# Kernel optimization log

Measured on AMD Instinct MI355X. Metric: run time of the kernel, lower is better.

The kernel has to match this reference:

```python
import jax, jax.numpy as jnp
import numpy as np

N_NODES = 100000
N_EDGES = 1600000
N_FEAT = 128
N_GRAPHS = 256
N_CLASSES = 2
BN_EPS = 1e-5


def _glorot(key, shape):
    lim = float(np.sqrt(6.0 / (shape[0] + shape[1])))
    return jax.random.uniform(key, shape, jnp.float32, -lim, lim)


def setup_inputs() -> dict:
    key = jax.random.key(0)
    ks = jax.random.split(key, 16)
    x = jax.random.normal(ks[0], (N_NODES, N_FEAT), jnp.float32)
    edge_index = jax.random.randint(ks[1], (2, N_EDGES), 0, N_NODES, jnp.int64)
    batch = jnp.sort(jax.random.randint(ks[2], (N_NODES,), 0, N_GRAPHS, jnp.int64))
    dims = [(N_FEAT, 16), (16, 32), (32, 64), (64, 50)]
    params = {}
    for i, (di, do) in enumerate(dims):
        params[f"W{i+1}"] = _glorot(ks[3 + i], (di, do))
        params[f"b{i+1}"] = jnp.zeros((do,), jnp.float32)
    params["bn_gamma"] = jnp.ones((50,), jnp.float32)
    params["bn_beta"] = jnp.zeros((50,), jnp.float32)
    params["fc1_W"] = _glorot(ks[8], (50, 30))
    params["fc1_b"] = jnp.zeros((30,), jnp.float32)
    params["fc2_W"] = _glorot(ks[9], (30, 20))
    params["fc2_b"] = jnp.zeros((20,), jnp.float32)
    params["fc3_W"] = _glorot(ks[10], (20, N_CLASSES))
    params["fc3_b"] = jnp.zeros((N_CLASSES,), jnp.float32)
    return {"x": x, "edge_index": edge_index, "batch": batch, **params}


def _gcn(x, W, b, src, dst):
    # GCNConv with normalize=False: out_i = sum_{(j->i) in E} (x_j @ W) + b
    h = x @ W                                   # [N, d_out]
    agg = jax.ops.segment_sum(h[src], dst, num_segments=N_NODES)
    return agg + b


def reference(x, edge_index, batch,
              W1, b1, W2, b2, W3, b3, W4, b4,
              bn_gamma, bn_beta,
              fc1_W, fc1_b, fc2_W, fc2_b, fc3_W, fc3_b):
    src, dst = edge_index[0], edge_index[1]
    lrelu = lambda v: jax.nn.leaky_relu(v, 0.01)
    h = lrelu(_gcn(x, W1, b1, src, dst))
    h = lrelu(_gcn(h, W2, b2, src, dst))
    h = lrelu(_gcn(h, W3, b3, src, dst))
    h = _gcn(h, W4, b4, src, dst)
    # BatchNorm over the node dimension (training-style batch stats, biased var)
    mu = jnp.mean(h, axis=0)
    var = jnp.mean((h - mu) ** 2, axis=0)
    h = lrelu((h - mu) * jax.lax.rsqrt(var + BN_EPS) * bn_gamma + bn_beta)
    # global_add_pool over graphs
    g = jax.ops.segment_sum(h, batch, num_segments=N_GRAPHS)   # [G, 50]
    g = lrelu(g @ fc1_W + fc1_b)   # dropout inactive (eval)
    g = lrelu(g @ fc2_W + fc2_b)
    g = g @ fc3_W + fc3_b
    return jax.nn.log_softmax(g, axis=-1)
```

## Files before the change

### kernel.cpp

```cpp
#include <hip/hip_runtime.h>

#define N_NODES 100000
#define N_EDGES 1600000
#define N_GRAPHS 256
#define NBKT 196
#define BKT_CAP 16384
#define BCHUNKS 391
#define MM1_BLOCKS 3125
#define A_BLOCKS (BCHUNKS + MM1_BLOCKS)

__device__ __forceinline__ float lrelu(float v) { return v > 0.f ? v : 0.01f * v; }

__device__ __forceinline__ unsigned short f2bf(float f) {
    unsigned int u = __float_as_uint(f);
    return (unsigned short)((u + 0x7FFFu + ((u >> 16) & 1u)) >> 16);
}
__device__ __forceinline__ float bf2f(unsigned short h) {
    return __uint_as_float(((unsigned int)h) << 16);
}
__device__ __forceinline__ float blo(unsigned int v) { return __uint_as_float(v << 16); }
__device__ __forceinline__ float bhi(unsigned int v) { return __uint_as_float(v & 0xFFFF0000u); }

__global__ void bucket_and_mm1(const int* __restrict__ src, const int* __restrict__ dst,
                               int* __restrict__ bucketCnt, unsigned int* __restrict__ bkt,
                               const float* __restrict__ x, const float* __restrict__ W1,
                               unsigned short* __restrict__ T1) {
    __shared__ float lds[32 * 132 + 128 * 16];
    int bid = blockIdx.x;
    int tid = threadIdx.x;
    if (bid % 9 == 0) {
        int* lcnt = (int*)lds;
        int* loff = lcnt + 784;
        int* lcnt2 = loff + 784;
        int fi = bid / 9;
        for (int i = tid; i < 784; i += 256) { lcnt[i] = 0; lcnt2[i] = 0; }
        __syncthreads();
        int sub = tid & 3;
        int e0 = fi * 4096 + tid;
        int dcache[16], scache[16];
#pragma unroll
        for (int i = 0; i < 16; ++i) {
            int e = e0 + i * 256;
            if (e < N_EDGES) {
                dcache[i] = dst[e];
                scache[i] = src[e];
                atomicAdd(&lcnt[sub * 196 + (dcache[i] >> 9)], 1);
            }
        }
        __syncthreads();
        if (tid < NBKT) {
            int c0 = lcnt[tid], c1 = lcnt[196 + tid], c2 = lcnt[392 + tid], c3 = lcnt[588 + tid];
            int tot = c0 + c1 + c2 + c3;
            int goff = (tot > 0) ? atomicAdd(&bucketCnt[tid], tot) : 0;
            loff[tid] = goff;
            loff[196 + tid] = goff + c0;
            loff[392 + tid] = goff + c0 + c1;
            loff[588 + tid] = goff + c0 + c1 + c2;
        }
        __syncthreads();
#pragma unroll
        for (int i = 0; i < 16; ++i) {
            int e = e0 + i * 256;
            if (e < N_EDGES) {
                int d = dcache[i];
                int b = d >> 9;
                int pos = loff[sub * 196 + b] + atomicAdd(&lcnt2[sub * 196 + b], 1);
                if (pos < BKT_CAP)
                    bkt[(size_t)b * BKT_CAP + pos] =
                        ((unsigned int)(d & 511) << 17) | (unsigned int)scache[i];
            }
        }
    } else {
        int mb = bid - bid / 9 - 1;
        float* xs = lds;
        float* wsm = lds + 32 * 132;
        const int n0 = mb * 32;
        for (int i = tid; i < 128 * 16; i += 256) wsm[i] = W1[i];
        const float4* X4 = (const float4*)x;
        for (int i = tid; i < 32 * 32; i += 256) {
            int r2 = i >> 5, c = i & 31;
            ((float4*)(xs + r2 * 132))[c] = X4[(size_t)(n0 + r2) * 32 + c];
        }
        __syncthreads();
        int r2 = tid >> 3, jp = tid & 7;
        float a0 = 0.f, a1 = 0.f;
        const float4* xr4 = (const float4*)(xs + r2 * 132);
#pragma unroll
        for (int k4 = 0; k4 < 32; ++k4) {
            float4 xv = xr4[k4];
            float2 w0 = *(const float2*)(wsm + (4 * k4 + 0) * 16 + 2 * jp);
            float2 w1 = *(const float2*)(wsm + (4 * k4 + 1) * 16 + 2 * jp);
            float2 w2 = *(const float2*)(wsm + (4 * k4 + 2) * 16 + 2 * jp);
            float2 w3 = *(const float2*)(wsm + (4 * k4 + 3) * 16 + 2 * jp);
            a0 = fmaf(xv.x, w0.x, a0); a1 = fmaf(xv.x, w0.y, a1);
            a0 = fmaf(xv.y, w1.x, a0); a1 = fmaf(xv.y, w1.y, a1);
            a0 = fmaf(xv.z, w2.x, a0); a1 = fmaf(xv.z, w2.y, a1);
            a0 = fmaf(xv.w, w3.x, a0); a1 = fmaf(xv.w, w3.y, a1);
        }
        ((unsigned int*)T1)[(size_t)(n0 + r2) * 8 + jp] = ((unsigned int)f2bf(a1) << 16) | f2bf(a0);
    }
}

__global__ void build_bucket(const unsigned int* __restrict__ bkt, const int* __restrict__ bucketCnt,
                             int* __restrict__ base, int* __restrict__ adj) {
    __shared__ int ldeg[512];
    __shared__ int lofs[512];
    __shared__ int ssum[256];
    int b = blockIdx.x;
    int tid = threadIdx.x;
    ssum[tid] = (tid < NBKT) ? bucketCnt[tid] : 0;
    __syncthreads();
    for (int off = 1; off < 256; off <<= 1) {
        int add = (tid >= off) ? ssum[tid - off] : 0;
        __syncthreads();
        ssum[tid] += add;
        __syncthreads();
    }
    int gbase = (b > 0) ? ssum[b - 1] : 0;
    int cnt = min(((b < NBKT) ? bucketCnt[b] : 0), BKT_CAP);
    int nstart = b * 512;
    int nn = min(512, N_NODES - nstart);
    const unsigned int* seg = bkt + (size_t)b * BKT_CAP;
    for (int i = tid; i < 512; i += 256) ldeg[i] = 0;
    __syncthreads();
    for (int e = tid; e < cnt; e += 256) atomicAdd(&ldeg[seg[e] >> 17], 1);
    __syncthreads();
    int a0 = ldeg[2 * tid], a1 = ldeg[2 * tid + 1];
    __syncthreads();
    ssum[tid] = a0 + a1;
    __syncthreads();
    for (int off = 1; off < 256; off <<= 1) {
        int add = (tid >= off) ? ssum[tid - off] : 0;
        __syncthreads();
        ssum[tid] += add;
        __syncthreads();
    }
    int prev = (tid > 0) ? ssum[tid - 1] : 0;
    lofs[2 * tid] = prev;
    lofs[2 * tid + 1] = prev + a0;
    __syncthreads();
    for (int i = tid; i < nn; i += 256) base[nstart + i] = gbase + lofs[i];
    if (b == 0 && tid == 0) base[N_NODES] = N_EDGES;
    for (int i = tid; i < 512; i += 256) ldeg[i] = 0;
    __syncthreads();
    for (int e = tid; e < cnt; e += 256) {
        unsigned int v = seg[e];
        int dl = (int)(v >> 17);
        int pos = atomicAdd(&ldeg[dl], 1);
        adj[gbase + lofs[dl] + pos] = (int)(v & 0x1FFFFu);
    }
}

template <int DIN, int DOUT, int ROWS, bool BIAS, bool RELU>
__global__ void matmul_rt(const unsigned int* __restrict__ X2, const float* __restrict__ W,
                          unsigned short* __restrict__ T, const float* __restrict__ bias) {
    constexpr int PAIRS = DOUT / 2;
    constexpr int PT = (PAIRS + 3) / 4;
    constexpr int RT = ROWS / 4;
    constexpr int XST = DIN + 1;
    __shared__ float xs[ROWS * XST];
    __shared__ float wsm[DIN * DOUT + 8];
    const int n0 = blockIdx.x * ROWS;
    const bool full = (n0 + ROWS <= N_NODES);
    int tid = threadIdx.x;
    for (int i = tid; i < DIN * DOUT; i += 256) wsm[i] = W[i];
    constexpr int V = DIN / 2;
    for (int i = tid; i < ROWS * V; i += 256) {
        int r = i / V, c = i - r * V;
        int node = n0 + r;
        unsigned int v = (full || node < N_NODES) ? X2[(size_t)node * V + c] : 0u;
        xs[r * XST + 2 * c]     = blo(v);
        xs[r * XST + 2 * c + 1] = bhi(v);
    }
    __syncthreads();
    if (tid >= RT * PT) return;
    int rt = tid / PT, pt = tid - rt * PT;
    const float* xr0 = xs + (rt * 4) * XST;
    const float* wp = wsm + 2 * (pt * 4);
    float2 acc[4][4];
#pragma unroll
    for (int i = 0; i < 4; ++i)
#pragma unroll
        for (int j = 0; j < 4; ++j) acc[i][j] = make_float2(0.f, 0.f);
#pragma unroll 4
    for (int k = 0; k < DIN; ++k) {
        float xv0 = xr0[k];
        float xv1 = xr0[XST + k];
        float xv2 = xr0[2 * XST + k];
        float xv3 = xr0[3 * XST + k];
        const float* wr = wp + k * DOUT;
        float2 w0 = *(const float2*)(wr);
        float2 w1 = *(const float2*)(wr + 2);
        float2 w2 = *(const float2*)(wr + 4);
        float2 w3 = *(const float2*)(wr + 6);
        acc[0][0].x = fmaf(xv0, w0.x, acc[0][0].x); acc[0][0].y = fmaf(xv0, w0.y, acc[0][0].y);
        acc[0][1].x = fmaf(xv0, w1.x, acc[0][1].x); acc[0][1].y = fmaf(xv0, w1.y, acc[0][1].y);
        acc[0][2].x = fmaf(xv0, w2.x, acc[0][2].x); acc[0][2].y = fmaf(xv0, w2.y, acc[0][2].y);
        acc[0][3].x = fmaf(xv0, w3.x, acc[0][3].x); acc[0][3].y = fmaf(xv0, w3.y, acc[0][3].y);
        acc[1][0].x = fmaf(xv1, w0.x, acc[1][0].x); acc[1][0].y = fmaf(xv1, w0.y, acc[1][0].y);
        acc[1][1].x = fmaf(xv1, w1.x, acc[1][1].x); acc[1][1].y = fmaf(xv1, w1.y, acc[1][1].y);
        acc[1][2].x = fmaf(xv1, w2.x, acc[1][2].x); acc[1][2].y = fmaf(xv1, w2.y, acc[1][2].y);
        acc[1][3].x = fmaf(xv1, w3.x, acc[1][3].x); acc[1][3].y = fmaf(xv1, w3.y, acc[1][3].y);
        acc[2][0].x = fmaf(xv2, w0.x, acc[2][0].x); acc[2][0].y = fmaf(xv2, w0.y, acc[2][0].y);
        acc[2][1].x = fmaf(xv2, w1.x, acc[2][1].x); acc[2][1].y = fmaf(xv2, w1.y, acc[2][1].y);
        acc[2][2].x = fmaf(xv2, w2.x, acc[2][2].x); acc[2][2].y = fmaf(xv2, w2.y, acc[2][2].y);
        acc[2][3].x = fmaf(xv2, w3.x, acc[2][3].x); acc[2][3].y = fmaf(xv2, w3.y, acc[2][3].y);
        acc[3][0].x = fmaf(xv3, w0.x, acc[3][0].x); acc[3][0].y = fmaf(xv3, w0.y, acc[3][0].y);
        acc[3][1].x = fmaf(xv3, w1.x, acc[3][1].x); acc[3][1].y = fmaf(xv3, w1.y, acc[3][1].y);
        acc[3][2].x = fmaf(xv3, w2.x, acc[3][2].x); acc[3][2].y = fmaf(xv3, w2.y, acc[3][2].y);
        acc[3][3].x = fmaf(xv3, w3.x, acc[3][3].x); acc[3][3].y = fmaf(xv3, w3.y, acc[3][3].y);
    }
    unsigned int* Tu = (unsigned int*)T;
#pragma unroll
    for (int i = 0; i < 4; ++i) {
        int node = n0 + rt * 4 + i;
        if (full || node < N_NODES) {
#pragma unroll
            for (int j = 0; j < 4; ++j) {
                int jp = pt * 4 + j;
                if (PAIRS % 4 == 0 || jp < PAIRS) {
                    float a0 = acc[i][j].x, a1 = acc[i][j].y;
                    if (BIAS) { a0 += bias[2 * jp]; a1 += bias[2 * jp + 1]; }
                    if (RELU) { a0 = lrelu(a0); a1 = lrelu(a1); }
                    Tu[(size_t)node * PAIRS + jp] = ((unsigned int)f2bf(a1) << 16) | f2bf(a0);
                }
            }
        }
    }
}

template <int DOUT, bool BIAS, bool RELU>
__global__ void gather_agg_bf16(const unsigned short* __restrict__ T, const int* __restrict__ base,
                                const int* __restrict__ adj, const float* __restrict__ b,
                                unsigned short* __restrict__ out) {
    constexpr int PAIRS = DOUT / 2;
    int gi = blockIdx.x * 256 + threadIdx.x;
    int node = gi / PAIRS;
    int j = gi - node * PAIRS;
    if (node >= N_NODES) return;
    const unsigned int* Tu = (const unsigned int*)T;
    int e0 = base[node], e1 = base[node + 1];
    float a0 = 0.f, a1 = 0.f, c0 = 0.f, c1 = 0.f;
    int k = e0;
    for (; k + 7 < e1; k += 8) {
        int s0 = adj[k], s1 = adj[k + 1], s2 = adj[k + 2], s3 = adj[k + 3];
        int s4 = adj[k + 4], s5 = adj[k + 5], s6 = adj[k + 6], s7 = adj[k + 7];
        unsigned int v0 = Tu[(size_t)s0 * PAIRS + j];
        unsigned int v1 = Tu[(size_t)s1 * PAIRS + j];
        unsigned int v2 = Tu[(size_t)s2 * PAIRS + j];
        unsigned int v3 = Tu[(size_t)s3 * PAIRS + j];
        unsigned int v4 = Tu[(size_t)s4 * PAIRS + j];
        unsigned int v5 = Tu[(size_t)s5 * PAIRS + j];
        unsigned int v6 = Tu[(size_t)s6 * PAIRS + j];
        unsigned int v7 = Tu[(size_t)s7 * PAIRS + j];
        a0 += blo(v0); a1 += bhi(v0);
        c0 += blo(v1); c1 += bhi(v1);
        a0 += blo(v2); a1 += bhi(v2);
        c0 += blo(v3); c1 += bhi(v3);
        a0 += blo(v4); a1 += bhi(v4);
        c0 += blo(v5); c1 += bhi(v5);
        a0 += blo(v6); a1 += bhi(v6);
        c0 += blo(v7); c1 += bhi(v7);
    }
    for (; k + 3 < e1; k += 4) {
        int s0 = adj[k], s1 = adj[k + 1], s2 = adj[k + 2], s3 = adj[k + 3];
        unsigned int v0 = Tu[(size_t)s0 * PAIRS + j];
        unsigned int v1 = Tu[(size_t)s1 * PAIRS + j];
        unsigned int v2 = Tu[(size_t)s2 * PAIRS + j];
        unsigned int v3 = Tu[(size_t)s3 * PAIRS + j];
        a0 += blo(v0); a1 += bhi(v0);
        c0 += blo(v1); c1 += bhi(v1);
        a0 += blo(v2); a1 += bhi(v2);
        c0 += blo(v3); c1 += bhi(v3);
    }
    for (; k < e1; ++k) {
        int s = adj[k];
        unsigned int v = Tu[(size_t)s * PAIRS + j];
        a0 += blo(v); a1 += bhi(v);
    }
    a0 += c0; a1 += c1;
    if (BIAS) { a0 += b[2 * j]; a1 += b[2 * j + 1]; }
    if (RELU) { a0 = lrelu(a0); a1 = lrelu(a1); }
    ((unsigned int*)out)[(size_t)node * PAIRS + j] = ((unsigned int)f2bf(a1) << 16) | f2bf(a0);
}

__global__ void bn_partial_kernel(const unsigned short* __restrict__ H, float* __restrict__ sum,
                                  float* __restrict__ ssum) {
    int tid = threadIdx.x;
    int j = tid % 50;
    int sub = tid / 50;
    float s = 0.f, ss = 0.f;
    if (tid < 250) {
        for (int node = blockIdx.x * 5 + sub; node < N_NODES; node += gridDim.x * 5) {
            float v = bf2f(H[(size_t)node * 50 + j]);
            s += v;
            ss += v * v;
        }
    }
    __shared__ float ls[256], lss[256];
    ls[tid] = s;
    lss[tid] = ss;
    __syncthreads();
    if (tid < 50) {
        float a = ls[tid] + ls[tid + 50] + ls[tid + 100] + ls[tid + 150] + ls[tid + 200];
        float c = lss[tid] + lss[tid + 50] + lss[tid + 100] + lss[tid + 150] + lss[tid + 200];
        atomicAdd(&sum[tid], a);
        atomicAdd(&ssum[tid], c);
    }
}

__global__ void setup_kernel(const int* __restrict__ batch, int* __restrict__ bounds,
                             int* __restrict__ bucketCnt, float* __restrict__ bnsum,
                             float* __restrict__ bnssum) {
    int tid = threadIdx.x;
    if (blockIdx.x == 0) {
        bucketCnt[tid] = 0;
    } else if (tid < 64) {
        bnsum[tid] = 0.f;
        bnssum[tid] = 0.f;
    }
    int g = blockIdx.x * 256 + tid;
    if (g > N_GRAPHS) return;
    int lo = 0, hi = N_NODES;
    while (lo < hi) {
        int mid = (lo + hi) >> 1;
        if (batch[mid] < g) lo = mid + 1; else hi = mid;
    }
    bounds[g] = lo;
}

__global__ void pool_seg_kernel(const unsigned short* __restrict__ H, const int* __restrict__ bounds,
                                const float* __restrict__ bnsum, const float* __restrict__ bnssum,
                                const float* __restrict__ gamma, const float* __restrict__ beta,
                                float* __restrict__ G) {
    int g = blockIdx.x;
    int s = bounds[g], e = bounds[g + 1];
    int tid = threadIdx.x;
    int j = tid % 50;
    int sub = tid / 50;
    float acc = 0.f;
    if (tid < 250) {
        float m = bnsum[j] / (float)N_NODES;
        float var = bnssum[j] / (float)N_NODES - m * m;
        float rs = rsqrtf(fmaxf(var, 0.f) + 1e-5f);
        float scale = rs * gamma[j];
        float shift = beta[j] - m * scale;
        for (int n = s + sub; n < e; n += 5) {
            float v = fmaf(bf2f(H[(size_t)n * 50 + j]), scale, shift);
            acc += lrelu(v);
        }
    }
    __shared__ float ls[256];
    ls[tid] = acc;
    __syncthreads();
    if (tid < 50) {
        G[g * 50 + tid] = ls[tid] + ls[tid + 50] + ls[tid + 100] + ls[tid + 150] + ls[tid + 200];
    }
}

__global__ void mlp_kernel(const float* __restrict__ G,
                           const float* __restrict__ fc1W, const float* __restrict__ fc1b,
                           const float* __restrict__ fc2W, const float* __restrict__ fc2b,
                           const float* __restrict__ fc3W, const float* __restrict__ fc3b,
                           float* __restrict__ out) {
    __shared__ float lw[2192];
    int tid = threadIdx.x;
    for (int i = tid; i < 1500; i += 256) lw[i] = fc1W[i];
    for (int i = tid; i < 30; i += 256) lw[1500 + i] = fc1b[i];
    for (int i = tid; i < 600; i += 256) lw[1530 + i] = fc2W[i];
    for (int i = tid; i < 20; i += 256) lw[2130 + i] = fc2b[i];
    for (int i = tid; i < 40; i += 256) lw[2150 + i] = fc3W[i];
    for (int i = tid; i < 2; i += 256) lw[2190 + i] = fc3b[i];
    __syncthreads();
    int g = blockIdx.x * 32 + tid;
    if (tid >= 32 || g >= N_GRAPHS) return;
    float a[50];
#pragma unroll
    for (int k = 0; k < 50; ++k) a[k] = G[g * 50 + k];
    float h1[30];
#pragma unroll
    for (int j = 0; j < 30; ++j) {
        float acc = lw[1500 + j];
#pragma unroll
        for (int k = 0; k < 50; ++k) acc = fmaf(a[k], lw[k * 30 + j], acc);
        h1[j] = lrelu(acc);
    }
    float h2[20];
#pragma unroll
    for (int j = 0; j < 20; ++j) {
        float acc = lw[2130 + j];
#pragma unroll
        for (int k = 0; k < 30; ++k) acc = fmaf(h1[k], lw[1530 + k * 20 + j], acc);
        h2[j] = lrelu(acc);
    }
    float z0 = lw[2190], z1 = lw[2191];
#pragma unroll
    for (int k = 0; k < 20; ++k) {
        z0 = fmaf(h2[k], lw[2150 + k * 2 + 0], z0);
        z1 = fmaf(h2[k], lw[2150 + k * 2 + 1], z1);
    }
    float m = fmaxf(z0, z1);
    float lse = m + logf(expf(z0 - m) + expf(z1 - m));
    out[g * 2 + 0] = z0 - lse;
    out[g * 2 + 1] = z1 - lse;
}

extern "C" void kernel_launch(void* const* d_in, const int* in_sizes, int n_in,
                              void* d_out, int out_size, void* d_ws, size_t ws_size,
                              hipStream_t stream) {
    const float* x     = (const float*)d_in[0];
    const int*   ei    = (const int*)d_in[1];
    const int*   batch = (const int*)d_in[2];
    const float* W1 = (const float*)d_in[3];  const float* b1 = (const float*)d_in[4];
    const float* W2 = (const float*)d_in[5];  const float* b2 = (const float*)d_in[6];
    const float* W3 = (const float*)d_in[7];  const float* b3 = (const float*)d_in[8];
    const float* W4 = (const float*)d_in[9];  const float* b4 = (const float*)d_in[10];
    const float* bng = (const float*)d_in[11]; const float* bnb = (const float*)d_in[12];
    const float* fc1W = (const float*)d_in[13]; const float* fc1b = (const float*)d_in[14];
    const float* fc2W = (const float*)d_in[15]; const float* fc2b = (const float*)d_in[16];
    const float* fc3W = (const float*)d_in[17]; const float* fc3b = (const float*)d_in[18];

    const int* src = ei;
    const int* dst = ei + N_EDGES;

    char* w = (char*)d_ws;
    unsigned short* bufA = (unsigned short*)w;      w += (size_t)6400000 * 2;
    unsigned short* bufB = (unsigned short*)w;      w += (size_t)6400000 * 2;
    int*   adj  = (int*)w;                          w += (size_t)N_EDGES * 4;
    unsigned int* bkt = (unsigned int*)w;           w += (size_t)NBKT * BKT_CAP * 4;
    int*   base = (int*)w;                          w += (size_t)(N_NODES + 1) * 4;
    int*   bucketCnt = (int*)w;                     w += 256 * 4;
    float* bnsum = (float*)w;                       w += 64 * 4;
    float* bnssum = (float*)w;                      w += 64 * 4;
    int*   bounds = (int*)w;                        w += (N_GRAPHS + 1) * 4;
    float* G    = (float*)w;                        w += (size_t)N_GRAPHS * 50 * 4;

    dim3 blk(256);

    setup_kernel<<<2, 256, 0, stream>>>(batch, bounds, bucketCnt, bnsum, bnssum);

    bucket_and_mm1<<<A_BLOCKS, blk, 0, stream>>>(src, dst, bucketCnt, bkt, x, W1, bufA);

    build_bucket<<<NBKT, blk, 0, stream>>>(bkt, bucketCnt, base, adj);

    gather_agg_bf16<16, true, true><<<(N_NODES * 8 + 255) / 256, blk, 0, stream>>>(bufA, base, adj, b1, bufB);

    gather_agg_bf16<16, false, false><<<(N_NODES * 8 + 255) / 256, blk, 0, stream>>>(bufB, base, adj, nullptr, bufA);
    matmul_rt<16, 32, 256, true, true><<<(N_NODES + 255) / 256, blk, 0, stream>>>((const unsigned int*)bufA, W2, bufB, b2);

    gather_agg_bf16<32, false, false><<<(N_NODES * 16 + 255) / 256, blk, 0, stream>>>(bufB, base, adj, nullptr, bufA);
    matmul_rt<32, 64, 128, true, true><<<(N_NODES + 127) / 128, blk, 0, stream>>>((const unsigned int*)bufA, W3, bufB, b3);

    matmul_rt<64, 50, 128, false, false><<<(N_NODES + 127) / 128, blk, 0, stream>>>((const unsigned int*)bufB, W4, bufA, nullptr);
    gather_agg_bf16<50, true, false><<<(N_NODES * 25 + 255) / 256, blk, 0, stream>>>(bufA, base, adj, b4, bufB);

    bn_partial_kernel<<<256, blk, 0, stream>>>(bufB, bnsum, bnssum);

    pool_seg_kernel<<<N_GRAPHS, blk, 0, stream>>>(bufB, bounds, bnsum, bnssum, bng, bnb, G);

    mlp_kernel<<<8, 256, 0, stream>>>(G, fc1W, fc1b, fc2W, fc2b, fc3W, fc3b, (float*)d_out);
}
```

Measured before the change: 282.3 us.

## Overlap the first matmul with CSR build instead of edge bucketing; unroll gather deeper

Edge bucketing now runs alone in its own kernel with smaller per-block chunks, twice as many blocks. The first-layer matmul is interleaved with the per-bucket CSR build (one build block every 17), so the dense matmul hides the latency of the atomic-heavy build step. The gather kernel's main loop now issues 16 neighbour loads per iteration instead of 8 to raise memory-level parallelism, at the cost of more registers. Kernel count stays the same, but the work is split differently across the first two launches.

```diff
diff --git a/kernel.cpp b/kernel.cpp
--- a/kernel.cpp
+++ b/kernel.cpp
@@ -5,9 +5,9 @@
 #define N_GRAPHS 256
 #define NBKT 196
 #define BKT_CAP 16384
-#define BCHUNKS 391
+#define B_BLOCKS 782
 #define MM1_BLOCKS 3125
-#define A_BLOCKS (BCHUNKS + MM1_BLOCKS)
+#define BM_BLOCKS (NBKT + MM1_BLOCKS)
 
 __device__ __forceinline__ float lrelu(float v) { return v > 0.f ? v : 0.01f * v; }
 
@@ -21,57 +21,105 @@
 __device__ __forceinline__ float blo(unsigned int v) { return __uint_as_float(v << 16); }
 __device__ __forceinline__ float bhi(unsigned int v) { return __uint_as_float(v & 0xFFFF0000u); }
 
-__global__ void bucket_and_mm1(const int* __restrict__ src, const int* __restrict__ dst,
-                               int* __restrict__ bucketCnt, unsigned int* __restrict__ bkt,
-                               const float* __restrict__ x, const float* __restrict__ W1,
-                               unsigned short* __restrict__ T1) {
+__global__ void bucket_only(const int* __restrict__ src, const int* __restrict__ dst,
+                            int* __restrict__ bucketCnt, unsigned int* __restrict__ bkt) {
+    __shared__ int lcnt[784], loff[784], lcnt2[784];
+    int fi = blockIdx.x;
+    int tid = threadIdx.x;
+    for (int i = tid; i < 784; i += 256) { lcnt[i] = 0; lcnt2[i] = 0; }
+    __syncthreads();
+    int sub = tid & 3;
+    int e0 = fi * 2048 + tid;
+    int dcache[8], scache[8];
+#pragma unroll
+    for (int i = 0; i < 8; ++i) {
+        int e = e0 + i * 256;
+        if (e < N_EDGES) {
+            dcache[i] = dst[e];
+            scache[i] = src[e];
+            atomicAdd(&lcnt[sub * 196 + (dcache[i] >> 9)], 1);
+        }
+    }
+    __syncthreads();
+    if (tid < NBKT) {
+        int c0 = lcnt[tid], c1 = lcnt[196 + tid], c2 = lcnt[392 + tid], c3 = lcnt[588 + tid];
+        int tot = c0 + c1 + c2 + c3;
+        int goff = (tot > 0) ? atomicAdd(&bucketCnt[tid], tot) : 0;
+        loff[tid] = goff;
+        loff[196 + tid] = goff + c0;
+        loff[392 + tid] = goff + c0 + c1;
+        loff[588 + tid] = goff + c0 + c1 + c2;
+    }
+    __syncthreads();
+#pragma unroll
+    for (int i = 0; i < 8; ++i) {
+        int e = e0 + i * 256;
+        if (e < N_EDGES) {
+            int d = dcache[i];
+            int b = d >> 9;
+            int pos = loff[sub * 196 + b] + atomicAdd(&lcnt2[sub * 196 + b], 1);
+            if (pos < BKT_CAP)
+                bkt[(size_t)b * BKT_CAP + pos] =
+                    ((unsigned int)(d & 511) << 17) | (unsigned int)scache[i];
+        }
+    }
+}
+
+__global__ void build_and_mm1(const unsigned int* __restrict__ bkt, const int* __restrict__ bucketCnt,
+                              int* __restrict__ base, int* __restrict__ adj,
+                              const float* __restrict__ x, const float* __restrict__ W1,
+                              unsigned short* __restrict__ T1) {
     __shared__ float lds[32 * 132 + 128 * 16];
     int bid = blockIdx.x;
     int tid = threadIdx.x;
-    if (bid % 9 == 0) {
-        int* lcnt = (int*)lds;
-        int* loff = lcnt + 784;
-        int* lcnt2 = loff + 784;
-        int fi = bid / 9;
-        for (int i = tid; i < 784; i += 256) { lcnt[i] = 0; lcnt2[i] = 0; }
-        __syncthreads();
-        int sub = tid & 3;
-        int e0 = fi * 4096 + tid;
-        int dcache[16], scache[16];
-#pragma unroll
-        for (int i = 0; i < 16; ++i) {
-            int e = e0 + i * 256;
-            if (e < N_EDGES) {
-                dcache[i] = dst[e];
-                scache[i] = src[e];
-                atomicAdd(&lcnt[sub * 196 + (dcache[i] >> 9)], 1);
-            }
-        }
-        __syncthreads();
-        if (tid < NBKT) {
-            int c0 = lcnt[tid], c1 = lcnt[196 + tid], c2 = lcnt[392 + tid], c3 = lcnt[588 + tid];
-            int tot = c0 + c1 + c2 + c3;
-            int goff = (tot > 0) ? atomicAdd(&bucketCnt[tid], tot) : 0;
-            loff[tid] = goff;
-            loff[196 + tid] = goff + c0;
-            loff[392 + tid] = goff + c0 + c1;
-            loff[588 + tid] = goff + c0 + c1 + c2;
-        }
-        __syncthreads();
-#pragma unroll
-        for (int i = 0; i < 16; ++i) {
-            int e = e0 + i * 256;
-            if (e < N_EDGES) {
-                int d = dcache[i];
-                int b = d >> 9;
-                int pos = loff[sub * 196 + b] + atomicAdd(&lcnt2[sub * 196 + b], 1);
-                if (pos < BKT_CAP)
-                    bkt[(size_t)b * BKT_CAP + pos] =
-                        ((unsigned int)(d & 511) << 17) | (unsigned int)scache[i];
-            }
+    if (bid % 17 == 0) {
+        int* ldeg = (int*)lds;
+        int* lofs = ldeg + 512;
+        int* ssum = lofs + 512;
+        int b = bid / 17;
+        ssum[tid] = (tid < NBKT) ? bucketCnt[tid] : 0;
+        __syncthreads();
+        for (int off = 1; off < 256; off <<= 1) {
+            int add = (tid >= off) ? ssum[tid - off] : 0;
+            __syncthreads();
+            ssum[tid] += add;
+            __syncthreads();
+        }
+        int gbase = (b > 0) ? ssum[b - 1] : 0;
+        int cnt = min(bucketCnt[b], BKT_CAP);
+        int nstart = b * 512;
+        int nn = min(512, N_NODES - nstart);
+        const unsigned int* seg = bkt + (size_t)b * BKT_CAP;
+        for (int i = tid; i < 512; i += 256) ldeg[i] = 0;
+        __syncthreads();
+        for (int e = tid; e < cnt; e += 256) atomicAdd(&ldeg[seg[e] >> 17], 1);
+        __syncthreads();
+        int a0 = ldeg[2 * tid], a1 = ldeg[2 * tid + 1];
+        __syncthreads();
+        ssum[tid] = a0 + a1;
+        __syncthreads();
+        for (int off = 1; off < 256; off <<= 1) {
+            int add = (tid >= off) ? ssum[tid - off] : 0;
+            __syncthreads();
+            ssum[tid] += add;
+            __syncthreads();
+        }
+        int prev = (tid > 0) ? ssum[tid - 1] : 0;
+        lofs[2 * tid] = prev;
+        lofs[2 * tid + 1] = prev + a0;
+        __syncthreads();
+        for (int i = tid; i < nn; i += 256) base[nstart + i] = gbase + lofs[i];
+        if (b == 0 && tid == 0) base[N_NODES] = N_EDGES;
+        for (int i = tid; i < 512; i += 256) ldeg[i] = 0;
+        __syncthreads();
+        for (int e = tid; e < cnt; e += 256) {
+            unsigned int v = seg[e];
+            int dl = (int)(v >> 17);
+            int pos = atomicAdd(&ldeg[dl], 1);
+            adj[gbase + lofs[dl] + pos] = (int)(v & 0x1FFFFu);
         }
     } else {
-        int mb = bid - bid / 9 - 1;
+        int mb = bid - bid / 17 - 1;
         float* xs = lds;
         float* wsm = lds + 32 * 132;
         const int n0 = mb * 32;
@@ -98,56 +146,6 @@
             a0 = fmaf(xv.w, w3.x, a0); a1 = fmaf(xv.w, w3.y, a1);
         }
         ((unsigned int*)T1)[(size_t)(n0 + r2) * 8 + jp] = ((unsigned int)f2bf(a1) << 16) | f2bf(a0);
-    }
-}
-
-__global__ void build_bucket(const unsigned int* __restrict__ bkt, const int* __restrict__ bucketCnt,
-                             int* __restrict__ base, int* __restrict__ adj) {
-    __shared__ int ldeg[512];
-    __shared__ int lofs[512];
-    __shared__ int ssum[256];
-    int b = blockIdx.x;
-    int tid = threadIdx.x;
-    ssum[tid] = (tid < NBKT) ? bucketCnt[tid] : 0;
-    __syncthreads();
-    for (int off = 1; off < 256; off <<= 1) {
-        int add = (tid >= off) ? ssum[tid - off] : 0;
-        __syncthreads();
-        ssum[tid] += add;
-        __syncthreads();
-    }
-    int gbase = (b > 0) ? ssum[b - 1] : 0;
-    int cnt = min(((b < NBKT) ? bucketCnt[b] : 0), BKT_CAP);
-    int nstart = b * 512;
-    int nn = min(512, N_NODES - nstart);
-    const unsigned int* seg = bkt + (size_t)b * BKT_CAP;
-    for (int i = tid; i < 512; i += 256) ldeg[i] = 0;
-    __syncthreads();
-    for (int e = tid; e < cnt; e += 256) atomicAdd(&ldeg[seg[e] >> 17], 1);
-    __syncthreads();
-    int a0 = ldeg[2 * tid], a1 = ldeg[2 * tid + 1];
-    __syncthreads();
-    ssum[tid] = a0 + a1;
-    __syncthreads();
-    for (int off = 1; off < 256; off <<= 1) {
-        int add = (tid >= off) ? ssum[tid - off] : 0;
-        __syncthreads();
-        ssum[tid] += add;
-        __syncthreads();
-    }
-    int prev = (tid > 0) ? ssum[tid - 1] : 0;
-    lofs[2 * tid] = prev;
-    lofs[2 * tid + 1] = prev + a0;
-    __syncthreads();
-    for (int i = tid; i < nn; i += 256) base[nstart + i] = gbase + lofs[i];
-    if (b == 0 && tid == 0) base[N_NODES] = N_EDGES;
-    for (int i = tid; i < 512; i += 256) ldeg[i] = 0;
-    __syncthreads();
-    for (int e = tid; e < cnt; e += 256) {
-        unsigned int v = seg[e];
-        int dl = (int)(v >> 17);
-        int pos = atomicAdd(&ldeg[dl], 1);
-        adj[gbase + lofs[dl] + pos] = (int)(v & 0x1FFFFu);
     }
 }
 
@@ -242,25 +240,18 @@
     int e0 = base[node], e1 = base[node + 1];
     float a0 = 0.f, a1 = 0.f, c0 = 0.f, c1 = 0.f;
     int k = e0;
-    for (; k + 7 < e1; k += 8) {
-        int s0 = adj[k], s1 = adj[k + 1], s2 = adj[k + 2], s3 = adj[k + 3];
-        int s4 = adj[k + 4], s5 = adj[k + 5], s6 = adj[k + 6], s7 = adj[k + 7];
-        unsigned int v0 = Tu[(size_t)s0 * PAIRS + j];
-        unsigned int v1 = Tu[(size_t)s1 * PAIRS + j];
-        unsigned int v2 = Tu[(size_t)s2 * PAIRS + j];
-        unsigned int v3 = Tu[(size_t)s3 * PAIRS + j];
-        unsigned int v4 = Tu[(size_t)s4 * PAIRS + j];
-        unsigned int v5 = Tu[(size_t)s5 * PAIRS + j];
-        unsigned int v6 = Tu[(size_t)s6 * PAIRS + j];
-        unsigned int v7 = Tu[(size_t)s7 * PAIRS + j];
-        a0 += blo(v0); a1 += bhi(v0);
-        c0 += blo(v1); c1 += bhi(v1);
-        a0 += blo(v2); a1 += bhi(v2);
-        c0 += blo(v3); c1 += bhi(v3);
-        a0 += blo(v4); a1 += bhi(v4);
-        c0 += blo(v5); c1 += bhi(v5);
-        a0 += blo(v6); a1 += bhi(v6);
-        c0 += blo(v7); c1 += bhi(v7);
+    for (; k + 15 < e1; k += 16) {
+        int s[16];
+#pragma unroll
+        for (int t = 0; t < 16; ++t) s[t] = adj[k + t];
+        unsigned int v[16];
+#pragma unroll
+        for (int t = 0; t < 16; ++t) v[t] = Tu[(size_t)s[t] * PAIRS + j];
+#pragma unroll
+        for (int t = 0; t < 16; ++t) {
+            if (t & 1) { c0 += blo(v[t]); c1 += bhi(v[t]); }
+            else       { a0 += blo(v[t]); a1 += bhi(v[t]); }
+        }
     }
     for (; k + 3 < e1; k += 4) {
         int s0 = adj[k], s1 = adj[k + 1], s2 = adj[k + 2], s3 = adj[k + 3];
@@ -439,9 +430,9 @@
 
     setup_kernel<<<2, 256, 0, stream>>>(batch, bounds, bucketCnt, bnsum, bnssum);
 
-    bucket_and_mm1<<<A_BLOCKS, blk, 0, stream>>>(src, dst, bucketCnt, bkt, x, W1, bufA);
-
-    build_bucket<<<NBKT, blk, 0, stream>>>(bkt, bucketCnt, base, adj);
+    bucket_only<<<B_BLOCKS, blk, 0, stream>>>(src, dst, bucketCnt, bkt);
+
+    build_and_mm1<<<BM_BLOCKS, blk, 0, stream>>>(bkt, bucketCnt, base, adj, x, W1, bufA);
 
     gather_agg_bf16<16, true, true><<<(N_NODES * 8 + 255) / 256, blk, 0, stream>>>(bufA, base, adj, b1, bufB);
 
```

After: 306.5 us. 8.6% more time.
